# Kernel optimization log

Hardware: AMD Instinct MI355X
Metric: run time of the kernel (lower is better)

Reference implementation:

```python
import jax, jax.numpy as jnp
import numpy as np

N_NODES = 100000
N_EDGES = 1600000
IN_FEAT = 128
HEADS = 4
OUT_FEAT = 16
ALPHA = 0.2  # LeakyReLU negative slope


def setup_inputs() -> dict:
    key = jax.random.key(0)
    k1, k2, k3, k4, k5 = jax.random.split(key, 5)
    x = jax.random.normal(k1, (N_NODES, IN_FEAT), dtype=jnp.float32)
    edge_index = jax.random.randint(k2, (2, N_EDGES), 0, N_NODES, dtype=jnp.int64)
    # xavier_uniform with gain=1.414
    gain = 1.414
    lim_W = gain * np.sqrt(6.0 / (IN_FEAT + HEADS * OUT_FEAT))
    W = jax.random.uniform(k3, (IN_FEAT, HEADS * OUT_FEAT), minval=-lim_W, maxval=lim_W, dtype=jnp.float32)
    lim_a = gain * np.sqrt(6.0 / (HEADS + OUT_FEAT))
    a_src = jax.random.uniform(k4, (HEADS, OUT_FEAT), minval=-lim_a, maxval=lim_a, dtype=jnp.float32)
    a_dst = jax.random.uniform(k5, (HEADS, OUT_FEAT), minval=-lim_a, maxval=lim_a, dtype=jnp.float32)
    return {"x": x, "edge_index": edge_index, "W": W, "a_src": a_src, "a_dst": a_dst}


def reference(x, edge_index, W, a_src, a_dst):
    N = x.shape[0]
    H, F = a_src.shape
    src, dst = edge_index[0], edge_index[1]

    h = (x @ W).reshape(N, H, F)                 # [N, H, F]
    att_src = jnp.sum(h * a_src, axis=-1)        # [N, H]
    att_dst = jnp.sum(h * a_dst, axis=-1)        # [N, H]

    e = jax.nn.leaky_relu(att_src[src] + att_dst[dst], negative_slope=ALPHA)  # [E, H]

    # segment softmax over edges grouped by dst
    e_max = jax.ops.segment_max(e, dst, num_segments=N)   # [N, H]
    e_max = jnp.where(jnp.isfinite(e_max), e_max, 0.0)    # nodes with no in-edges
    ex = jnp.exp(e - e_max[dst])                           # [E, H]
    denom = jax.ops.segment_sum(ex, dst, num_segments=N)  # [N, H]
    alpha = ex / (denom[dst] + 1e-16)                      # [E, H]
    # dropout: inference mode (training=False) -> identity

    messages = h[src] * alpha[:, :, None]                  # [E, H, F]
    out = jax.ops.segment_sum(messages, dst, num_segments=N)  # [N, H, F]

    out = out.reshape(N, H * F)  # concat=True
    out = jax.nn.elu(out)
    return out
```

## Files before the change

kernel.cpp:

```cpp
#include <hip/hip_runtime.h>


#define NEG_SLOPE 0.2f
#define BSHIFT 9
#define BNODES 512
#define CH 2048
#define QNODES 64
#define BCAP 9216
#define SCAP 1536
#define SCAPC 256

typedef __bf16 bf16x8 __attribute__((ext_vector_type(8)));
typedef float  f32x4  __attribute__((ext_vector_type(4)));

static __device__ __forceinline__ unsigned f2b(float f) {
    union { float f; unsigned u; } v; v.f = f;
    return (v.u + 0x7fffu + ((v.u >> 16) & 1u)) >> 16;
}
static __device__ __forceinline__ float u2f(unsigned u) {
    union { unsigned u32; float f; } v; v.u32 = u; return v.f;
}

struct SmemGemm { bf16x8 Wswz[20][64]; };
struct SmemScat {
    int cnt[256], lo[256], gpos[256], cur[256], sm[256];
    int2 staged[CH];
};
union SmemU { SmemGemm g; SmemScat s; };

__global__ __launch_bounds__(256) void fused_gemm_bscatter_kernel(
    const float* __restrict__ x,
    const float* __restrict__ W,
    const float* __restrict__ a_src,
    const float* __restrict__ a_dst,
    unsigned short* __restrict__ h_out,
    float* __restrict__ att_s_o,
    float* __restrict__ att_d_o,
    const int* __restrict__ src, const int* __restrict__ dst,
    int* __restrict__ gcur, int* __restrict__ pairs,
    int N, int E, int blocksS)
{
    __shared__ SmemU u;
    int t = threadIdx.x;

    if (blockIdx.x < blocksS) {
        int base = blockIdx.x * CH;
        int nloc = min(CH, E - base);

        u.s.cnt[t] = 0;
        __syncthreads();
        for (int i = t; i < nloc; i += 256)
            atomicAdd(&u.s.cnt[dst[base + i] >> BSHIFT], 1);
        __syncthreads();

        int v = u.s.cnt[t];
        u.s.sm[t] = v;
        __syncthreads();
        #pragma unroll
        for (int off = 1; off < 256; off <<= 1) {
            int w = (t >= off) ? u.s.sm[t - off] : 0;
            __syncthreads();
            u.s.sm[t] += w;
            __syncthreads();
        }
        u.s.lo[t] = u.s.sm[t] - v;
        u.s.cur[t] = u.s.lo[t];
        u.s.gpos[t] = (v > 0) ? t * BCAP + atomicAdd(&gcur[t], v) : 0;
        __syncthreads();

        for (int i = t; i < nloc; i += 256) {
            int d = dst[base + i];
            int s = src[base + i];
            int b = d >> BSHIFT;
            int k = atomicAdd(&u.s.cur[b], 1);
            u.s.staged[k] = make_int2((s << BSHIFT) | (d & (BNODES - 1)), b);
        }
        __syncthreads();

        for (int i = t; i < nloc; i += 256) {
            int2 p = u.s.staged[i];
            int pos = u.s.gpos[p.y] + (i - u.s.lo[p.y]);
            if (pos < (p.y + 1) * BCAP)
                pairs[pos] = p.x;
        }
        return;
    }

    int bid = blockIdx.x - blocksS;

    for (int i = t; i < 8192; i += 256) {
        int k = i >> 6, n = i & 63;
        __bf16* dp = (__bf16*)&u.g.Wswz[((n >> 4) << 2) | (k >> 5)]
                                       [(((k >> 3) & 3) << 4) | (n & 15)];
        dp[k & 7] = (__bf16)W[i];
    }
    for (int i = t; i < 1024; i += 256) {
        int k = i >> 3, c7 = i & 7;
        int hd = c7 & 3;
        const float* aa = (c7 < 4) ? a_src : a_dst;
        float sum = 0.f;
        #pragma unroll
        for (int f = 0; f < 16; ++f)
            sum = fmaf(W[k * 64 + hd * 16 + f], aa[hd * 16 + f], sum);
        __bf16* dp = (__bf16*)&u.g.Wswz[16 + (k >> 5)][(((k >> 3) & 3) << 4) | c7];
        dp[k & 7] = (__bf16)sum;
        __bf16* dz = (__bf16*)&u.g.Wswz[16 + (k >> 5)][(((k >> 3) & 3) << 4) | (8 + c7)];
        dz[k & 7] = (__bf16)0.f;
    }
    __syncthreads();

    int wave = t >> 6;
    int lane = t & 63;
    int col = lane & 15, quad = lane >> 4;
    int node_base = (bid * 4 + wave) * 16;
    int arow = min(node_base + col, N - 1);
    const float* xp = x + arow * 128;

    bf16x8 af[4];
    #pragma unroll
    for (int tt = 0; tt < 4; ++tt) {
        float4 xa = *(const float4*)(xp + tt * 32 + quad * 8);
        float4 xb = *(const float4*)(xp + tt * 32 + quad * 8 + 4);
        bf16x8 f;
        f[0] = (__bf16)xa.x; f[1] = (__bf16)xa.y;
        f[2] = (__bf16)xa.z; f[3] = (__bf16)xa.w;
        f[4] = (__bf16)xb.x; f[5] = (__bf16)xb.y;
        f[6] = (__bf16)xb.z; f[7] = (__bf16)xb.w;
        af[tt] = f;
    }

    f32x4 acc[4], accA;
    #pragma unroll
    for (int cb = 0; cb < 4; ++cb) {
        acc[cb] = (f32x4){0.f, 0.f, 0.f, 0.f};
        #pragma unroll
        for (int tt = 0; tt < 4; ++tt)
            acc[cb] = __builtin_amdgcn_mfma_f32_16x16x32_bf16(
                af[tt], u.g.Wswz[(cb << 2) | tt][lane], acc[cb], 0, 0, 0);
    }
    accA = (f32x4){0.f, 0.f, 0.f, 0.f};
    #pragma unroll
    for (int tt = 0; tt < 4; ++tt)
        accA = __builtin_amdgcn_mfma_f32_16x16x32_bf16(
            af[tt], u.g.Wswz[16 + tt][lane], accA, 0, 0, 0);

    #pragma unroll
    for (int cb = 0; cb < 4; ++cb) {
        #pragma unroll
        for (int r = 0; r < 4; ++r) {
            int node = node_base + quad * 4 + r;
            if (node < N)
                h_out[node * 64 + cb * 16 + col] = (unsigned short)f2b(acc[cb][r]);
        }
    }
    if (col < 8) {
        #pragma unroll
        for (int r = 0; r < 4; ++r) {
            int node = node_base + quad * 4 + r;
            if (node < N) {
                if (col < 4) att_s_o[(node << 2) | col] = accA[r];
                else         att_d_o[(node << 2) | (col - 4)] = accA[r];
            }
        }
    }
}

__global__ __launch_bounds__(256) void sliceshuffle_kernel(
    const int* __restrict__ pairs, const int* __restrict__ gcur,
    int* __restrict__ pairs2, int* __restrict__ scnt)
{
    __shared__ int cur8[8];
    int blk = blockIdx.x, t = threadIdx.x;
    int b = blk >> 3, chunk = blk & 7;
    int cnt = min(gcur[b], BCAP);
    int clo = (cnt * chunk) >> 3;
    int chi = (cnt * (chunk + 1)) >> 3;
    int lane = t & 63;
    unsigned long long below = (lane == 0) ? 0ull : ((~0ull) >> (64 - lane));
    const int* pb = pairs + (size_t)b * BCAP;
    if (t < 8) cur8[t] = 0;
    __syncthreads();

    for (int i = clo + t; i < chi; i += 256) {
        int p = pb[i];
        int sl = (p >> 6) & 7;
        int pos = 0;
        #pragma unroll
        for (int s = 0; s < 8; ++s) {
            unsigned long long m = __ballot(sl == s);
            if (sl == s) {
                int rank = __popcll(m & below);
                int b0 = 0;
                if (rank == 0) b0 = atomicAdd(&cur8[s], (int)__popcll(m));
                b0 = __shfl(b0, (int)(__ffsll((long long)m) - 1), 64);
                pos = b0 + rank;
            }
        }
        if (pos < SCAPC)
            pairs2[((size_t)((((b << 3) | sl) << 3) | chunk)) * SCAPC + pos] = p;
    }
    __syncthreads();
    if (t < 8) scnt[((((b << 3) | t) << 3) | chunk)] = min(cur8[t], SCAPC);
}

__global__ __launch_bounds__(256, 8) void bucket_csr_agg_kernel(
    const int* __restrict__ pairs2,
    const int* __restrict__ scnt,
    const float* __restrict__ att_s,
    const float* __restrict__ att_d,
    const unsigned short* __restrict__ hmat,
    float* __restrict__ out,
    int N)
{
    __shared__ int sorted[SCAP];
    __shared__ int cnt[QNODES], rs[QNODES + 1], cur[QNODES], sm[QNODES];
    __shared__ int scn[8];
    __shared__ float attd[QNODES * 4];

    int blk = blockIdx.x, t = threadIdx.x;
    int b = blk >> 3, s8 = blk & 7;
    int node_lo = (b << BSHIFT) + (s8 << 6);
    if (node_lo >= N) return;
    int nn = min(QNODES, N - node_lo);

    if (t < QNODES) cnt[t] = 0;
    if (t < 8) scn[t] = scnt[(blk << 3) | t];
    for (int i = t; i < (nn << 2); i += 256)
        attd[i] = att_d[(node_lo << 2) + i];
    __syncthreads();

    const int* sbase = pairs2 + ((size_t)blk << 3) * SCAPC;
    #pragma unroll
    for (int c = 0; c < 8; ++c) {
        int cn = scn[c];
        const int* seg = sbase + c * SCAPC;
        for (int i = t; i < cn; i += 256)
            atomicAdd(&cnt[seg[i] & (QNODES - 1)], 1);
    }
    __syncthreads();

    int v = (t < QNODES) ? cnt[t] : 0;
    if (t < QNODES) sm[t] = v;
    __syncthreads();
    #pragma unroll
    for (int off = 1; off < QNODES; off <<= 1) {
        int u = (t >= off && t < QNODES) ? sm[t - off] : 0;
        __syncthreads();
        if (t < QNODES) sm[t] += u;
        __syncthreads();
    }
    if (t < QNODES) {
        int x = sm[t] - v; rs[t] = x; cur[t] = x;
        if (t == QNODES - 1) rs[QNODES] = sm[t];
    }
    __syncthreads();

    #pragma unroll
    for (int c = 0; c < 8; ++c) {
        int cn = scn[c];
        const int* seg = sbase + c * SCAPC;
        for (int i = t; i < cn; i += 256) {
            int p = seg[i];
            int k = atomicAdd(&cur[p & (QNODES - 1)], 1);
            if (k < SCAP) sorted[k] = p >> BSHIFT;
        }
    }
    __syncthreads();

    int q = t & 7;
    int h = q >> 1;
    int nclamp = N - 1;

    for (int pass = 0; pass < 2; ++pass) {
        int node = (pass << 5) + (t >> 3);
        if (node >= nn) continue;
        int beg = rs[node];
        int deg = rs[node + 1] - beg;
        float ad = attd[(node << 2) | h];

        float a0 = 0.f, a1 = 0.f, a2 = 0.f, a3 = 0.f;
        float a4 = 0.f, a5 = 0.f, a6 = 0.f, a7 = 0.f, l = 0.f;
        int d1 = deg - 1;
        for (int e0 = 0; e0 < deg; e0 += 4) {
            int s0 = min(sorted[beg + min(e0 + 0, d1)], nclamp);
            int s1 = min(sorted[beg + min(e0 + 1, d1)], nclamp);
            int s2 = min(sorted[beg + min(e0 + 2, d1)], nclamp);
            int s3 = min(sorted[beg + min(e0 + 3, d1)], nclamp);
            float t0 = att_s[(s0 << 2) | h];
            float t1 = att_s[(s1 << 2) | h];
            float t2 = att_s[(s2 << 2) | h];
            float t3 = att_s[(s3 << 2) | h];
            uint4 hp0 = *(const uint4*)(hmat + (s0 << 6) + (q << 3));
            uint4 hp1 = *(const uint4*)(hmat + (s1 << 6) + (q << 3));
            uint4 hp2 = *(const uint4*)(hmat + (s2 << 6) + (q << 3));
            uint4 hp3 = *(const uint4*)(hmat + (s3 << 6) + (q << 3));
            float av0 = t0 + ad; av0 = fmaxf(av0, NEG_SLOPE * av0);
            float av1 = t1 + ad; av1 = fmaxf(av1, NEG_SLOPE * av1);
            float av2 = t2 + ad; av2 = fmaxf(av2, NEG_SLOPE * av2);
            float av3 = t3 + ad; av3 = fmaxf(av3, NEG_SLOPE * av3);
            float w0 = __expf(av0);
            float w1 = (e0 + 1 < deg) ? __expf(av1) : 0.f;
            float w2 = (e0 + 2 < deg) ? __expf(av2) : 0.f;
            float w3 = (e0 + 3 < deg) ? __expf(av3) : 0.f;
            l += w0 + w1 + w2 + w3;
            a0 = fmaf(w0, u2f(hp0.x << 16), a0);
            a1 = fmaf(w0, u2f(hp0.x & 0xffff0000u), a1);
            a2 = fmaf(w0, u2f(hp0.y << 16), a2);
            a3 = fmaf(w0, u2f(hp0.y & 0xffff0000u), a3);
            a4 = fmaf(w0, u2f(hp0.z << 16), a4);
            a5 = fmaf(w0, u2f(hp0.z & 0xffff0000u), a5);
            a6 = fmaf(w0, u2f(hp0.w << 16), a6);
            a7 = fmaf(w0, u2f(hp0.w & 0xffff0000u), a7);
            a0 = fmaf(w1, u2f(hp1.x << 16), a0);
            a1 = fmaf(w1, u2f(hp1.x & 0xffff0000u), a1);
            a2 = fmaf(w1, u2f(hp1.y << 16), a2);
            a3 = fmaf(w1, u2f(hp1.y & 0xffff0000u), a3);
            a4 = fmaf(w1, u2f(hp1.z << 16), a4);
            a5 = fmaf(w1, u2f(hp1.z & 0xffff0000u), a5);
            a6 = fmaf(w1, u2f(hp1.w << 16), a6);
            a7 = fmaf(w1, u2f(hp1.w & 0xffff0000u), a7);
            a0 = fmaf(w2, u2f(hp2.x << 16), a0);
            a1 = fmaf(w2, u2f(hp2.x & 0xffff0000u), a1);
            a2 = fmaf(w2, u2f(hp2.y << 16), a2);
            a3 = fmaf(w2, u2f(hp2.y & 0xffff0000u), a3);
            a4 = fmaf(w2, u2f(hp2.z << 16), a4);
            a5 = fmaf(w2, u2f(hp2.z & 0xffff0000u), a5);
            a6 = fmaf(w2, u2f(hp2.w << 16), a6);
            a7 = fmaf(w2, u2f(hp2.w & 0xffff0000u), a7);
            a0 = fmaf(w3, u2f(hp3.x << 16), a0);
            a1 = fmaf(w3, u2f(hp3.x & 0xffff0000u), a1);
            a2 = fmaf(w3, u2f(hp3.y << 16), a2);
            a3 = fmaf(w3, u2f(hp3.y & 0xffff0000u), a3);
            a4 = fmaf(w3, u2f(hp3.z << 16), a4);
            a5 = fmaf(w3, u2f(hp3.z & 0xffff0000u), a5);
            a6 = fmaf(w3, u2f(hp3.w << 16), a6);
            a7 = fmaf(w3, u2f(hp3.w & 0xffff0000u), a7);
        }

        float rl = 1.0f / (l + 1e-16f);
        float4 v0, v1;
        v0.x = a0 * rl; v0.x = (v0.x > 0.f) ? v0.x : (__expf(v0.x) - 1.f);
        v0.y = a1 * rl; v0.y = (v0.y > 0.f) ? v0.y : (__expf(v0.y) - 1.f);
        v0.z = a2 * rl; v0.z = (v0.z > 0.f) ? v0.z : (__expf(v0.z) - 1.f);
        v0.w = a3 * rl; v0.w = (v0.w > 0.f) ? v0.w : (__expf(v0.w) - 1.f);
        v1.x = a4 * rl; v1.x = (v1.x > 0.f) ? v1.x : (__expf(v1.x) - 1.f);
        v1.y = a5 * rl; v1.y = (v1.y > 0.f) ? v1.y : (__expf(v1.y) - 1.f);
        v1.z = a6 * rl; v1.z = (v1.z > 0.f) ? v1.z : (__expf(v1.z) - 1.f);
        v1.w = a7 * rl; v1.w = (v1.w > 0.f) ? v1.w : (__expf(v1.w) - 1.f);
        float* op = out + ((size_t)(node_lo + node) << 6) + (q << 3);
        *(float4*)op = v0;
        *(float4*)(op + 4) = v1;
    }
}

extern "C" void kernel_launch(void* const* d_in, const int* in_sizes, int n_in,
                              void* d_out, int out_size, void* d_ws, size_t ws_size,
                              hipStream_t stream) {
    const float* x     = (const float*)d_in[0];
    const int*   ei    = (const int*)d_in[1];
    const float* W     = (const float*)d_in[2];
    const float* a_src = (const float*)d_in[3];
    const float* a_dst = (const float*)d_in[4];

    int N = in_sizes[0] / 128;
    int E = in_sizes[1] / 2;
    const int* src = ei;
    const int* dst = ei + E;
    int nb = (N + BNODES - 1) / BNODES;

    char* ws = (char*)d_ws;
    size_t off = 0;
    unsigned short* hmat = (unsigned short*)(ws + off); off += (size_t)N * 64 * 2;
    float* att_s = (float*)(ws + off);  off += (size_t)N * 4 * 4;
    float* att_d = (float*)(ws + off);  off += (size_t)N * 4 * 4;
    int* pairs    = (int*)(ws + off);   off += (size_t)nb * BCAP * 4;
    int* pairs2   = (int*)(ws + off);   off += (size_t)nb * 64 * SCAPC * 4;
    int* gcur     = (int*)(ws + off);   off += 256 * 4;
    int* scnt     = (int*)(ws + off);   off += (size_t)nb * 64 * 4;

    hipMemsetAsync(gcur, 0, 256 * 4, stream);

    int blocksS = (E + CH - 1) / CH;
    int gemmBlocks = (N + 63) / 64;
    fused_gemm_bscatter_kernel<<<blocksS + gemmBlocks, 256, 0, stream>>>(
        x, W, a_src, a_dst, hmat, att_s, att_d,
        src, dst, gcur, pairs, N, E, blocksS);

    sliceshuffle_kernel<<<nb * 8, 256, 0, stream>>>(pairs, gcur, pairs2, scnt);

    bucket_csr_agg_kernel<<<nb * 8, 256, 0, stream>>>(
        pairs2, scnt, att_s, att_d, hmat, (float*)d_out, N);
}
```

Before: 192.0 us.

## Merge three kernels into a persistent megakernel with software grid barriers

Replaces the three separate launches (fused GEMM/bucket scatter, slice shuffle, CSR aggregation) with one persistent kernel sized to full occupancy. Phases are separated by a two-level atomic grid barrier, and blocks loop over work units inside each phase. The aim is to remove kernel launch gaps and per-launch tail effects. In exchange it adds barrier spin cost and lower occupancy (launch bounds 256,4 with a union of shared-memory layouts). It also depends on every block being co-resident, and the old launch path is kept as a fallback.

Result: slower. 403.9 us (+110.3%).

```diff
diff --git a/kernel.cpp b/kernel.cpp
--- a/kernel.cpp
+++ b/kernel.cpp
@@ -9,9 +9,16 @@
 #define BCAP 9216
 #define SCAP 1536
 #define SCAPC 256
+#define L1W 64
 
 typedef __bf16 bf16x8 __attribute__((ext_vector_type(8)));
 typedef float  f32x4  __attribute__((ext_vector_type(4)));
+
+struct GBar {
+    int c1[L1W * 16];
+    int c2;  int pad1[15];
+    int gen; int pad2[15];
+};
 
 static __device__ __forceinline__ unsigned f2b(float f) {
     union { float f; unsigned u; } v; v.f = f;
@@ -21,77 +28,102 @@
     union { unsigned u32; float f; } v; v.u32 = u; return v.f;
 }
 
-struct SmemGemm { bf16x8 Wswz[20][64]; };
+static __device__ __forceinline__ void grid_barrier(GBar* gb) {
+    __syncthreads();
+    if (threadIdx.x == 0) {
+        int g = __hip_atomic_load(&gb->gen, __ATOMIC_ACQUIRE,
+                                  __HIP_MEMORY_SCOPE_AGENT);
+        __threadfence();
+        int gsz = (int)gridDim.x;
+        int i1 = (int)blockIdx.x & (L1W - 1);
+        int quota = (gsz - i1 + L1W - 1) / L1W;
+        if (atomicAdd(&gb->c1[i1 * 16], 1) == quota - 1) {
+            int nact = gsz < L1W ? gsz : L1W;
+            if (atomicAdd(&gb->c2, 1) == nact - 1) {
+                #pragma unroll 4
+                for (int k = 0; k < L1W; ++k) atomicExch(&gb->c1[k * 16], 0);
+                atomicExch(&gb->c2, 0);
+                __threadfence();
+                atomicAdd(&gb->gen, 1);
+            }
+        }
+        while (__hip_atomic_load(&gb->gen, __ATOMIC_ACQUIRE,
+                                 __HIP_MEMORY_SCOPE_AGENT) == g)
+            __builtin_amdgcn_s_sleep(8);
+        __threadfence();
+    }
+    __syncthreads();
+}
+
 struct SmemScat {
     int cnt[256], lo[256], gpos[256], cur[256], sm[256];
     int2 staged[CH];
 };
-union SmemU { SmemGemm g; SmemScat s; };
-
-__global__ __launch_bounds__(256) void fused_gemm_bscatter_kernel(
-    const float* __restrict__ x,
-    const float* __restrict__ W,
-    const float* __restrict__ a_src,
-    const float* __restrict__ a_dst,
-    unsigned short* __restrict__ h_out,
-    float* __restrict__ att_s_o,
-    float* __restrict__ att_d_o,
-    const int* __restrict__ src, const int* __restrict__ dst,
-    int* __restrict__ gcur, int* __restrict__ pairs,
-    int N, int E, int blocksS)
-{
-    __shared__ SmemU u;
+struct SmemGemm { bf16x8 Wswz[20][64]; };
+struct SmemAgg {
+    int sorted[SCAP];
+    int cnt[QNODES], rs[QNODES + 1], cur[QNODES], sm[QNODES];
+    int scn[8];
+    float attd[QNODES * 4];
+};
+struct SmemShuf { int cur8[8]; };
+union SmemU { SmemGemm g; SmemScat s; SmemAgg a; SmemShuf h; };
+
+static __device__ __forceinline__ void bscatter_unit(
+    SmemScat& S, int v, const int* __restrict__ src, const int* __restrict__ dst,
+    int* __restrict__ gcur, int* __restrict__ pairs, int E)
+{
     int t = threadIdx.x;
-
-    if (blockIdx.x < blocksS) {
-        int base = blockIdx.x * CH;
-        int nloc = min(CH, E - base);
-
-        u.s.cnt[t] = 0;
+    int base = v * CH;
+    int nloc = min(CH, E - base);
+
+    S.cnt[t] = 0;
+    __syncthreads();
+    for (int i = t; i < nloc; i += 256)
+        atomicAdd(&S.cnt[dst[base + i] >> BSHIFT], 1);
+    __syncthreads();
+
+    int vv = S.cnt[t];
+    S.sm[t] = vv;
+    __syncthreads();
+    #pragma unroll
+    for (int off = 1; off < 256; off <<= 1) {
+        int w = (t >= off) ? S.sm[t - off] : 0;
         __syncthreads();
-        for (int i = t; i < nloc; i += 256)
-            atomicAdd(&u.s.cnt[dst[base + i] >> BSHIFT], 1);
+        S.sm[t] += w;
         __syncthreads();
-
-        int v = u.s.cnt[t];
-        u.s.sm[t] = v;
-        __syncthreads();
-        #pragma unroll
-        for (int off = 1; off < 256; off <<= 1) {
-            int w = (t >= off) ? u.s.sm[t - off] : 0;
-            __syncthreads();
-            u.s.sm[t] += w;
-            __syncthreads();
-        }
-        u.s.lo[t] = u.s.sm[t] - v;
-        u.s.cur[t] = u.s.lo[t];
-        u.s.gpos[t] = (v > 0) ? t * BCAP + atomicAdd(&gcur[t], v) : 0;
-        __syncthreads();
-
-        for (int i = t; i < nloc; i += 256) {
-            int d = dst[base + i];
-            int s = src[base + i];
-            int b = d >> BSHIFT;
-            int k = atomicAdd(&u.s.cur[b], 1);
-            u.s.staged[k] = make_int2((s << BSHIFT) | (d & (BNODES - 1)), b);
-        }
-        __syncthreads();
-
-        for (int i = t; i < nloc; i += 256) {
-            int2 p = u.s.staged[i];
-            int pos = u.s.gpos[p.y] + (i - u.s.lo[p.y]);
-            if (pos < (p.y + 1) * BCAP)
-                pairs[pos] = p.x;
-        }
-        return;
-    }
-
-    int bid = blockIdx.x - blocksS;
-
+    }
+    S.lo[t] = S.sm[t] - vv;
+    S.cur[t] = S.lo[t];
+    S.gpos[t] = (vv > 0) ? t * BCAP + atomicAdd(&gcur[t], vv) : 0;
+    __syncthreads();
+
+    for (int i = t; i < nloc; i += 256) {
+        int d = dst[base + i];
+        int s = src[base + i];
+        int b = d >> BSHIFT;
+        int k = atomicAdd(&S.cur[b], 1);
+        S.staged[k] = make_int2((s << BSHIFT) | (d & (BNODES - 1)), b);
+    }
+    __syncthreads();
+
+    for (int i = t; i < nloc; i += 256) {
+        int2 p = S.staged[i];
+        int pos = S.gpos[p.y] + (i - S.lo[p.y]);
+        if (pos < (p.y + 1) * BCAP)
+            pairs[pos] = p.x;
+    }
+}
+
+static __device__ __forceinline__ void gemm_build_W(
+    SmemGemm& G, const float* __restrict__ W,
+    const float* __restrict__ a_src, const float* __restrict__ a_dst)
+{
+    int t = threadIdx.x;
     for (int i = t; i < 8192; i += 256) {
         int k = i >> 6, n = i & 63;
-        __bf16* dp = (__bf16*)&u.g.Wswz[((n >> 4) << 2) | (k >> 5)]
-                                       [(((k >> 3) & 3) << 4) | (n & 15)];
+        __bf16* dp = (__bf16*)&G.Wswz[((n >> 4) << 2) | (k >> 5)]
+                                     [(((k >> 3) & 3) << 4) | (n & 15)];
         dp[k & 7] = (__bf16)W[i];
     }
     for (int i = t; i < 1024; i += 256) {
@@ -102,17 +134,23 @@
         #pragma unroll
         for (int f = 0; f < 16; ++f)
             sum = fmaf(W[k * 64 + hd * 16 + f], aa[hd * 16 + f], sum);
-        __bf16* dp = (__bf16*)&u.g.Wswz[16 + (k >> 5)][(((k >> 3) & 3) << 4) | c7];
+        __bf16* dp = (__bf16*)&G.Wswz[16 + (k >> 5)][(((k >> 3) & 3) << 4) | c7];
         dp[k & 7] = (__bf16)sum;
-        __bf16* dz = (__bf16*)&u.g.Wswz[16 + (k >> 5)][(((k >> 3) & 3) << 4) | (8 + c7)];
+        __bf16* dz = (__bf16*)&G.Wswz[16 + (k >> 5)][(((k >> 3) & 3) << 4) | (8 + c7)];
         dz[k & 7] = (__bf16)0.f;
     }
-    __syncthreads();
-
+}
+
+static __device__ __forceinline__ void gemm_unit(
+    const SmemGemm& G, int v, const float* __restrict__ x,
+    unsigned short* __restrict__ h_out, float* __restrict__ att_s_o,
+    float* __restrict__ att_d_o, int N)
+{
+    int t = threadIdx.x;
     int wave = t >> 6;
     int lane = t & 63;
     int col = lane & 15, quad = lane >> 4;
-    int node_base = (bid * 4 + wave) * 16;
+    int node_base = (v * 4 + wave) * 16;
     int arow = min(node_base + col, N - 1);
     const float* xp = x + arow * 128;
 
@@ -136,13 +174,13 @@
         #pragma unroll
         for (int tt = 0; tt < 4; ++tt)
             acc[cb] = __builtin_amdgcn_mfma_f32_16x16x32_bf16(
-                af[tt], u.g.Wswz[(cb << 2) | tt][lane], acc[cb], 0, 0, 0);
+                af[tt], G.Wswz[(cb << 2) | tt][lane], acc[cb], 0, 0, 0);
     }
     accA = (f32x4){0.f, 0.f, 0.f, 0.f};
     #pragma unroll
     for (int tt = 0; tt < 4; ++tt)
         accA = __builtin_amdgcn_mfma_f32_16x16x32_bf16(
-            af[tt], u.g.Wswz[16 + tt][lane], accA, 0, 0, 0);
+            af[tt], G.Wswz[16 + tt][lane], accA, 0, 0, 0);
 
     #pragma unroll
     for (int cb = 0; cb < 4; ++cb) {
@@ -165,13 +203,13 @@
     }
 }
 
-__global__ __launch_bounds__(256) void sliceshuffle_kernel(
-    const int* __restrict__ pairs, const int* __restrict__ gcur,
-    int* __restrict__ pairs2, int* __restrict__ scnt)
-{
-    __shared__ int cur8[8];
-    int blk = blockIdx.x, t = threadIdx.x;
-    int b = blk >> 3, chunk = blk & 7;
+static __device__ __forceinline__ void shuffle_unit(
+    int* cur8, int v, const int* __restrict__ pairs,
+    const int* __restrict__ gcur, int* __restrict__ pairs2,
+    int* __restrict__ scnt)
+{
+    int t = threadIdx.x;
+    int b = v >> 3, chunk = v & 7;
     int cnt = min(gcur[b], BCAP);
     int clo = (cnt * chunk) >> 3;
     int chi = (cnt * (chunk + 1)) >> 3;
@@ -203,66 +241,59 @@
     if (t < 8) scnt[((((b << 3) | t) << 3) | chunk)] = min(cur8[t], SCAPC);
 }
 
-__global__ __launch_bounds__(256, 8) void bucket_csr_agg_kernel(
-    const int* __restrict__ pairs2,
-    const int* __restrict__ scnt,
-    const float* __restrict__ att_s,
-    const float* __restrict__ att_d,
-    const unsigned short* __restrict__ hmat,
-    float* __restrict__ out,
-    int N)
-{
-    __shared__ int sorted[SCAP];
-    __shared__ int cnt[QNODES], rs[QNODES + 1], cur[QNODES], sm[QNODES];
-    __shared__ int scn[8];
-    __shared__ float attd[QNODES * 4];
-
-    int blk = blockIdx.x, t = threadIdx.x;
+static __device__ __forceinline__ void agg_unit(
+    SmemAgg& A, int blk, const int* __restrict__ pairs2,
+    const int* __restrict__ scnt, const float* __restrict__ att_s,
+    const float* __restrict__ att_d, const unsigned short* __restrict__ hmat,
+    float* __restrict__ out, int N)
+{
+    int t = threadIdx.x;
     int b = blk >> 3, s8 = blk & 7;
     int node_lo = (b << BSHIFT) + (s8 << 6);
     if (node_lo >= N) return;
     int nn = min(QNODES, N - node_lo);
 
-    if (t < QNODES) cnt[t] = 0;
-    if (t < 8) scn[t] = scnt[(blk << 3) | t];
+    __syncthreads();
+    if (t < QNODES) A.cnt[t] = 0;
+    if (t < 8) A.scn[t] = scnt[(blk << 3) | t];
     for (int i = t; i < (nn << 2); i += 256)
-        attd[i] = att_d[(node_lo << 2) + i];
+        A.attd[i] = att_d[(node_lo << 2) + i];
     __syncthreads();
 
     const int* sbase = pairs2 + ((size_t)blk << 3) * SCAPC;
     #pragma unroll
     for (int c = 0; c < 8; ++c) {
-        int cn = scn[c];
+        int cn = A.scn[c];
         const int* seg = sbase + c * SCAPC;
         for (int i = t; i < cn; i += 256)
-            atomicAdd(&cnt[seg[i] & (QNODES - 1)], 1);
-    }
-    __syncthreads();
-
-    int v = (t < QNODES) ? cnt[t] : 0;
-    if (t < QNODES) sm[t] = v;
+            atomicAdd(&A.cnt[seg[i] & (QNODES - 1)], 1);
+    }
+    __syncthreads();
+
+    int v = (t < QNODES) ? A.cnt[t] : 0;
+    if (t < QNODES) A.sm[t] = v;
     __syncthreads();
     #pragma unroll
     for (int off = 1; off < QNODES; off <<= 1) {
-        int u = (t >= off && t < QNODES) ? sm[t - off] : 0;
+        int u = (t >= off && t < QNODES) ? A.sm[t - off] : 0;
         __syncthreads();
-        if (t < QNODES) sm[t] += u;
+        if (t < QNODES) A.sm[t] += u;
         __syncthreads();
     }
     if (t < QNODES) {
-        int x = sm[t] - v; rs[t] = x; cur[t] = x;
-        if (t == QNODES - 1) rs[QNODES] = sm[t];
+        int x = A.sm[t] - v; A.rs[t] = x; A.cur[t] = x;
+        if (t == QNODES - 1) A.rs[QNODES] = A.sm[t];
     }
     __syncthreads();
 
     #pragma unroll
     for (int c = 0; c < 8; ++c) {
-        int cn = scn[c];
+        int cn = A.scn[c];
         const int* seg = sbase + c * SCAPC;
         for (int i = t; i < cn; i += 256) {
             int p = seg[i];
-            int k = atomicAdd(&cur[p & (QNODES - 1)], 1);
-            if (k < SCAP) sorted[k] = p >> BSHIFT;
+            int k = atomicAdd(&A.cur[p & (QNODES - 1)], 1);
+            if (k < SCAP) A.sorted[k] = p >> BSHIFT;
         }
     }
     __syncthreads();
@@ -274,18 +305,18 @@
     for (int pass = 0; pass < 2; ++pass) {
         int node = (pass << 5) + (t >> 3);
         if (node >= nn) continue;
-        int beg = rs[node];
-        int deg = rs[node + 1] - beg;
-        float ad = attd[(node << 2) | h];
+        int beg = A.rs[node];
+        int deg = A.rs[node + 1] - beg;
+        float ad = A.attd[(node << 2) | h];
 
         float a0 = 0.f, a1 = 0.f, a2 = 0.f, a3 = 0.f;
         float a4 = 0.f, a5 = 0.f, a6 = 0.f, a7 = 0.f, l = 0.f;
         int d1 = deg - 1;
         for (int e0 = 0; e0 < deg; e0 += 4) {
-            int s0 = min(sorted[beg + min(e0 + 0, d1)], nclamp);
-            int s1 = min(sorted[beg + min(e0 + 1, d1)], nclamp);
-            int s2 = min(sorted[beg + min(e0 + 2, d1)], nclamp);
-            int s3 = min(sorted[beg + min(e0 + 3, d1)], nclamp);
+            int s0 = min(A.sorted[beg + min(e0 + 0, d1)], nclamp);
+            int s1 = min(A.sorted[beg + min(e0 + 1, d1)], nclamp);
+            int s2 = min(A.sorted[beg + min(e0 + 2, d1)], nclamp);
+            int s3 = min(A.sorted[beg + min(e0 + 3, d1)], nclamp);
             float t0 = att_s[(s0 << 2) | h];
             float t1 = att_s[(s1 << 2) | h];
             float t2 = att_s[(s2 << 2) | h];
@@ -353,6 +384,76 @@
     }
 }
 
+__global__ __launch_bounds__(256, 4) void mega_kernel(
+    const float* __restrict__ x, const float* __restrict__ W,
+    const float* __restrict__ a_src, const float* __restrict__ a_dst,
+    unsigned short* __restrict__ hmat, float* __restrict__ att_s,
+    float* __restrict__ att_d,
+    const int* __restrict__ src, const int* __restrict__ dst,
+    int* __restrict__ gcur, int* __restrict__ pairs,
+    int* __restrict__ pairs2, int* __restrict__ scnt,
+    float* __restrict__ out, GBar* __restrict__ gbar,
+    int N, int E, int blocksS, int gemmUnits, int aggUnits, int SB)
+{
+    __shared__ SmemU u;
+    int gsz = (int)gridDim.x;
+
+    if ((int)blockIdx.x < SB) {
+        for (int v = blockIdx.x; v < (unsigned)blocksS; v += SB)
+            bscatter_unit(u.s, v, src, dst, gcur, pairs, E);
+    } else {
+        gemm_build_W(u.g, W, a_src, a_dst);
+        __syncthreads();
+        int nG = gsz - SB;
+        for (int v = (int)blockIdx.x - SB; v < gemmUnits; v += nG)
+            gemm_unit(u.g, v, x, hmat, att_s, att_d, N);
+    }
+    grid_barrier(gbar);
+
+    for (int v = blockIdx.x; v < (unsigned)aggUnits; v += gsz)
+        shuffle_unit(u.h.cur8, v, pairs, gcur, pairs2, scnt);
+    grid_barrier(gbar);
+
+    for (int v = blockIdx.x; v < (unsigned)aggUnits; v += gsz)
+        agg_unit(u.a, v, pairs2, scnt, att_s, att_d, hmat, out, N);
+}
+
+__global__ __launch_bounds__(256) void fused_gemm_bscatter_kernel(
+    const float* __restrict__ x, const float* __restrict__ W,
+    const float* __restrict__ a_src, const float* __restrict__ a_dst,
+    unsigned short* __restrict__ h_out, float* __restrict__ att_s_o,
+    float* __restrict__ att_d_o,
+    const int* __restrict__ src, const int* __restrict__ dst,
+    int* __restrict__ gcur, int* __restrict__ pairs,
+    int N, int E, int blocksS)
+{
+    __shared__ SmemU u;
+    if ((int)blockIdx.x < blocksS) {
+        bscatter_unit(u.s, blockIdx.x, src, dst, gcur, pairs, E);
+        return;
+    }
+    gemm_build_W(u.g, W, a_src, a_dst);
+    __syncthreads();
+    gemm_unit(u.g, blockIdx.x - blocksS, x, h_out, att_s_o, att_d_o, N);
+}
+
+__global__ __launch_bounds__(256) void sliceshuffle_kernel(
+    const int* __restrict__ pairs, const int* __restrict__ gcur,
+    int* __restrict__ pairs2, int* __restrict__ scnt)
+{
+    __shared__ int cur8[8];
+    shuffle_unit(cur8, blockIdx.x, pairs, gcur, pairs2, scnt);
+}
+
+__global__ __launch_bounds__(256, 8) void bucket_csr_agg_kernel(
+    const int* __restrict__ pairs2, const int* __restrict__ scnt,
+    const float* __restrict__ att_s, const float* __restrict__ att_d,
+    const unsigned short* __restrict__ hmat, float* __restrict__ out, int N)
+{
+    __shared__ SmemAgg a;
+    agg_unit(a, blockIdx.x, pairs2, scnt, att_s, att_d, hmat, out, N);
+}
+
 extern "C" void kernel_launch(void* const* d_in, const int* in_sizes, int n_in,
                               void* d_out, int out_size, void* d_ws, size_t ws_size,
                               hipStream_t stream) {
@@ -376,18 +477,47 @@
     int* pairs    = (int*)(ws + off);   off += (size_t)nb * BCAP * 4;
     int* pairs2   = (int*)(ws + off);   off += (size_t)nb * 64 * SCAPC * 4;
     int* gcur     = (int*)(ws + off);   off += 256 * 4;
+    GBar* gbar    = (GBar*)(ws + off);  off += sizeof(GBar);
     int* scnt     = (int*)(ws + off);   off += (size_t)nb * 64 * 4;
-
-    hipMemsetAsync(gcur, 0, 256 * 4, stream);
-
-    int blocksS = (E + CH - 1) / CH;
-    int gemmBlocks = (N + 63) / 64;
-    fused_gemm_bscatter_kernel<<<blocksS + gemmBlocks, 256, 0, stream>>>(
-        x, W, a_src, a_dst, hmat, att_s, att_d,
-        src, dst, gcur, pairs, N, E, blocksS);
-
-    sliceshuffle_kernel<<<nb * 8, 256, 0, stream>>>(pairs, gcur, pairs2, scnt);
-
-    bucket_csr_agg_kernel<<<nb * 8, 256, 0, stream>>>(
-        pairs2, scnt, att_s, att_d, hmat, (float*)d_out, N);
-}
+    float* outp   = (float*)d_out;
+
+    int blocksS   = (E + CH - 1) / CH;
+    int gemmUnits = (N + 63) / 64;
+    int aggUnits  = nb * 8;
+
+    static int megaGrid = -1;
+    if (megaGrid == -1) {
+        megaGrid = 0;
+        int dev = 0;
+        hipGetDevice(&dev);
+        hipDeviceProp_t prop;
+        int occ = 0;
+        if (hipGetDeviceProperties(&prop, dev) == hipSuccess &&
+            hipOccupancyMaxActiveBlocksPerMultiprocessor(
+                &occ, mega_kernel, 256, 0) == hipSuccess && occ > 0)
+            megaGrid = occ * prop.multiProcessorCount;
+    }
+
+    hipMemsetAsync(gcur, 0, 256 * 4 + sizeof(GBar), stream);
+
+    if (megaGrid >= 256) {
+        int grid = megaGrid;
+        int maxU = blocksS + gemmUnits;
+        if (grid > maxU) grid = maxU;
+        int SB = (int)((long long)grid * blocksS / (blocksS + gemmUnits));
+        if (SB < 1) SB = 1;
+        if (SB > grid - 1) SB = grid - 1;
+        mega_kernel<<<grid, 256, 0, stream>>>(
+            x, W, a_src, a_dst, hmat, att_s, att_d, src, dst,
+            gcur, pairs, pairs2, scnt, outp, gbar,
+            N, E, blocksS, gemmUnits, aggUnits, SB);
+    } else {
+        fused_gemm_bscatter_kernel<<<blocksS + gemmUnits, 256, 0, stream>>>(
+            x, W, a_src, a_dst, hmat, att_s, att_d,
+            src, dst, gcur, pairs, N, E, blocksS);
+        sliceshuffle_kernel<<<aggUnits, 256, 0, stream>>>(pairs, gcur,
+                                                          pairs2, scnt);
+        bucket_csr_agg_kernel<<<aggUnits, 256, 0, stream>>>(
+            pairs2, scnt, att_s, att_d, hmat, outp, N);
+    }
+}
```
